# Kernel optimization log

Hardware: AMD Instinct MI355X
Metric: run time of the kernel (lower is better)

## Reference

```python
import jax, jax.numpy as jnp
import numpy as np

D = 120000   # sample_size
H1 = 600     # sample_size/200
H2 = 300     # sample_size/400
H3 = 200     # sample_size/600
DENSITY = 0.1  # sparselinear default connectivity
B = 512
EPS = 1e-5

_LAYER_SPECS = [(H1, D), (H1, H1), (H2, H1), (H3, H2), (H3, H3)]


def _make_idx(key, out_d, in_d, nnz):
    k1, k2 = jax.random.split(key)
    rows = jax.random.randint(k1, (nnz,), 0, out_d)
    cols = jax.random.randint(k2, (nnz,), 0, in_d)
    return jnp.stack([rows, cols]).astype(jnp.int32)


def setup_inputs() -> dict:
    key = jax.random.key(0)
    ks = jax.random.split(key, 32)
    inp = {"x": jax.random.normal(ks[0], (B, D), jnp.float32)}
    for i, (o, ii) in enumerate(_LAYER_SPECS, 1):
        nnz = int(DENSITY * o * ii)
        scale = 1.0 / np.sqrt(DENSITY * ii)  # kaiming-like fan-in scaling on nonzeros
        inp[f"idx{i}"] = _make_idx(ks[3 * i], o, ii, nnz)
        inp[f"val{i}"] = jax.random.normal(ks[3 * i + 1], (nnz,), jnp.float32) * scale
        inp[f"b{i}"] = jnp.zeros((o,), jnp.float32)
    for j, d in enumerate([H1, H2, H3], 1):
        inp[f"g{j}"] = jnp.ones((d,), jnp.float32)
        inp[f"be{j}"] = jnp.zeros((d,), jnp.float32)
    return inp


def _sp_linear(x, idx, vals, bias, out_d):
    # COO sparse linear: y = x @ W^T + b, W scattered from (row, col, val)
    in_d = x.shape[1]
    W = jnp.zeros((out_d, in_d), x.dtype).at[idx[0], idx[1]].add(vals)
    return x @ W.T + bias


def _bn(x, g, b):
    # BatchNorm1d, training mode: biased batch variance
    m = x.mean(axis=0)
    v = x.var(axis=0)
    return (x - m) * jax.lax.rsqrt(v + EPS) * g + b


def reference(x, idx1, val1, b1, idx2, val2, b2, idx3, val3, b3,
              idx4, val4, b4, idx5, val5, b5,
              g1, be1, g2, be2, g3, be3):
    h = jax.nn.silu(_bn(_sp_linear(x, idx1, val1, b1, H1), g1, be1))
    h = jax.nn.silu(_sp_linear(h, idx2, val2, b2, H1))
    h = jax.nn.silu(_bn(_sp_linear(h, idx3, val3, b3, H2), g2, be2))
    h = jax.nn.silu(_bn(_sp_linear(h, idx4, val4, b4, H3), g3, be3))
    return _sp_linear(h, idx5, val5, b5, H3)
```

## Files before the change

### kernel.cpp

```cpp
#include <hip/hip_runtime.h>

typedef unsigned short ushort_t;
typedef unsigned int uint_t;

typedef __bf16 bf16x8 __attribute__((ext_vector_type(8)));
typedef float  floatx4 __attribute__((ext_vector_type(4)));

#define AS3 __attribute__((address_space(3)))
#define AS1 __attribute__((address_space(1)))

#define BATCH 512
#define D_IN  120000
#define N1P   640
#define N2P   640
#define N3P   320
#define N4P   256
#define N5P   256

static constexpr long O_W1 = 0;
static constexpr long SZ_W1 = 640L * 120000 * 2;
static constexpr long O_W2 = O_W1 + SZ_W1;
static constexpr long SZ_W2 = 640L * 640 * 4;
static constexpr long O_W3 = O_W2 + SZ_W2;
static constexpr long SZ_W3 = 320L * 640 * 4;
static constexpr long O_W4 = O_W3 + SZ_W3;
static constexpr long SZ_W4 = 256L * 320 * 4;
static constexpr long O_W5 = O_W4 + SZ_W4;
static constexpr long SZ_W5 = 256L * 256 * 4;
static constexpr long O_Y1 = O_W5 + SZ_W5;
static constexpr long SZ_Y1 = 512L * 640 * 4;
static constexpr long ZERO_BYTES = O_Y1 + SZ_Y1;
static constexpr long O_XB = ZERO_BYTES;
static constexpr long SZ_XB = 512L * 120000 * 2;
static constexpr long O_H1 = O_XB;
static constexpr long O_H2 = O_H1 + 512L * 640 * 4;
static constexpr long O_Y3 = O_H2 + 512L * 640 * 4;
static constexpr long O_H3 = O_Y3 + 512L * 320 * 4;
static constexpr long O_Y4 = O_H3 + 512L * 320 * 4;
static constexpr long O_H4 = O_Y4 + 512L * 256 * 4;

__device__ __forceinline__ ushort_t f2bf(float f) {
    union { float f; uint_t u; } x;
    x.f = f;
    uint_t u = x.u;
    return (ushort_t)((u + 0x7FFFu + ((u >> 16) & 1u)) >> 16);
}
__device__ __forceinline__ float bf2f(ushort_t h) {
    union { uint_t u; float f; } x;
    x.u = ((uint_t)h) << 16;
    return x.f;
}
__device__ __forceinline__ float silu_f(float z) {
    return z / (1.f + expf(-z));
}
__device__ __forceinline__ void load16_lds(const void* g, void* l) {
    __builtin_amdgcn_global_load_lds((const AS1 char*)g, (AS3 char*)l, 16, 0, 0);
}

__global__ void zero_f4(float4* __restrict__ p, long n4) {
    long stride = (long)gridDim.x * blockDim.x;
    for (long i = (long)blockIdx.x * blockDim.x + threadIdx.x; i < n4; i += stride)
        p[i] = make_float4(0.f, 0.f, 0.f, 0.f);
}

__global__ void cast_f32_bf16(const float* __restrict__ X, ushort_t* __restrict__ Xb, long n8) {
    long t = (long)blockIdx.x * blockDim.x + threadIdx.x;
    if (t >= n8) return;
    const float4* p = (const float4*)X + 2 * t;
    float4 a = p[0], b = p[1];
    union { ushort_t us[8]; uint4 v; } u;
    u.us[0] = f2bf(a.x); u.us[1] = f2bf(a.y); u.us[2] = f2bf(a.z); u.us[3] = f2bf(a.w);
    u.us[4] = f2bf(b.x); u.us[5] = f2bf(b.y); u.us[6] = f2bf(b.z); u.us[7] = f2bf(b.w);
    ((uint4*)Xb)[t] = u.v;
}

__global__ void scatter_bf16(const int* __restrict__ idx, const float* __restrict__ vals,
                             int nnz, ushort_t* __restrict__ W, int ldw) {
    int i = blockIdx.x * blockDim.x + threadIdx.x;
    if (i >= nnz) return;
    int r = idx[i];
    int c = idx[nnz + i];
    float v = vals[i];
    size_t e = (size_t)r * ldw + c;
    uint_t* word = (uint_t*)((char*)W + ((e * 2) & ~(size_t)3));
    bool hi = (e & 1);
    uint_t cur = *word, assumed;
    do {
        assumed = cur;
        ushort_t h = hi ? (ushort_t)(assumed >> 16) : (ushort_t)(assumed & 0xFFFFu);
        ushort_t nh = f2bf(bf2f(h) + v);
        uint_t nw = hi ? ((assumed & 0x0000FFFFu) | ((uint_t)nh << 16))
                       : ((assumed & 0xFFFF0000u) | (uint_t)nh);
        cur = atomicCAS(word, assumed, nw);
    } while (cur != assumed);
}

__global__ void scatter_f32(const int* __restrict__ idx, const float* __restrict__ vals,
                            int nnz, float* __restrict__ W, int ldw) {
    int i = blockIdx.x * blockDim.x + threadIdx.x;
    if (i >= nnz) return;
    atomicAdd(&W[(size_t)idx[i] * ldw + idx[nnz + i]], vals[i]);
}

__global__ __launch_bounds__(256) void gemm1(const ushort_t* __restrict__ X,
                                             const ushort_t* __restrict__ W,
                                             float* __restrict__ Y, int kChunk) {
    __shared__ ushort_t sA[128 * 32];
    __shared__ ushort_t sB[128 * 32];

    const int tile = blockIdx.x;
    const int bm = tile / 5, bn = tile % 5;
    const int ks = blockIdx.y * kChunk;
    const int iters = kChunk / 32;

    const int t = threadIdx.x;
    const int lane = t & 63;
    const int w = t >> 6;
    const int wm = w >> 1, wn = w & 1;

    const int c0 = w * 128 + lane;
    const int c1 = c0 + 64;
    const int rA0 = c0 >> 2, qA0 = c0 & 3;
    const int rA1 = c1 >> 2, qA1 = c1 & 3;

    const ushort_t* pa0 = X + (size_t)(bm * 128 + rA0) * D_IN + ks + qA0 * 8;
    const ushort_t* pa1 = X + (size_t)(bm * 128 + rA1) * D_IN + ks + qA1 * 8;
    const ushort_t* pb0 = W + (size_t)(bn * 128 + rA0) * D_IN + ks + qA0 * 8;
    const ushort_t* pb1 = W + (size_t)(bn * 128 + rA1) * D_IN + ks + qA1 * 8;

    ushort_t* la0 = sA + (size_t)(w * 128) * 8;
    ushort_t* la1 = sA + (size_t)(w * 128 + 64) * 8;
    ushort_t* lb0 = sB + (size_t)(w * 128) * 8;
    ushort_t* lb1 = sB + (size_t)(w * 128 + 64) * 8;

    const int i16 = lane & 15;
    const int qk = lane >> 4;
    const bf16x8* ap[4];
    const bf16x8* bp[4];
#pragma unroll
    for (int mi = 0; mi < 4; mi++)
        ap[mi] = (const bf16x8*)&sA[(size_t)(wm * 64 + mi * 16 + i16) * 32 + qk * 8];
#pragma unroll
    for (int ni = 0; ni < 4; ni++)
        bp[ni] = (const bf16x8*)&sB[(size_t)(wn * 64 + ni * 16 + i16) * 32 + qk * 8];

    floatx4 acc[4][4] = {};

    for (int it = 0; it < iters; ++it) {
        __syncthreads();
        load16_lds(pa0, la0);
        load16_lds(pa1, la1);
        load16_lds(pb0, lb0);
        load16_lds(pb1, lb1);
        pa0 += 32; pa1 += 32; pb0 += 32; pb1 += 32;
        __syncthreads();

        bf16x8 af[4], bfr[4];
#pragma unroll
        for (int mi = 0; mi < 4; mi++) af[mi] = *ap[mi];
#pragma unroll
        for (int ni = 0; ni < 4; ni++) bfr[ni] = *bp[ni];
#pragma unroll
        for (int mi = 0; mi < 4; mi++)
#pragma unroll
            for (int ni = 0; ni < 4; ni++)
                acc[mi][ni] = __builtin_amdgcn_mfma_f32_16x16x32_bf16(af[mi], bfr[ni], acc[mi][ni], 0, 0, 0);
    }

#pragma unroll
    for (int mi = 0; mi < 4; mi++) {
#pragma unroll
        for (int ni = 0; ni < 4; ni++) {
#pragma unroll
            for (int r = 0; r < 4; r++) {
                int row = bm * 128 + wm * 64 + mi * 16 + qk * 4 + r;
                int col = bn * 128 + wn * 64 + ni * 16 + i16;
                atomicAdd(&Y[(size_t)row * N1P + col], acc[mi][ni][r]);
            }
        }
    }
}

__global__ void bn_silu(const float* __restrict__ Y, int ld, int realN,
                        const float* __restrict__ g, const float* __restrict__ be,
                        float* __restrict__ H) {
    int j = blockIdx.x;
    int t = threadIdx.x;
    if (j >= realN) {
        for (int b = t; b < BATCH; b += 256) H[(size_t)b * ld + j] = 0.f;
        return;
    }
    float v0 = Y[(size_t)t * ld + j];
    float v1 = Y[(size_t)(t + 256) * ld + j];
    __shared__ float rs[256], rss[256];
    rs[t] = v0 + v1;
    rss[t] = v0 * v0 + v1 * v1;
    __syncthreads();
    for (int o = 128; o > 0; o >>= 1) {
        if (t < o) { rs[t] += rs[t + o]; rss[t] += rss[t + o]; }
        __syncthreads();
    }
    float mean = rs[0] * (1.f / 512.f);
    float var  = rss[0] * (1.f / 512.f) - mean * mean;
    float sc = rsqrtf(var + 1e-5f) * g[j];
    float sh = be[j] - mean * sc;
    H[(size_t)t * ld + j]         = silu_f(v0 * sc + sh);
    H[(size_t)(t + 256) * ld + j] = silu_f(v1 * sc + sh);
}

template <int ACT, int GUARD>
__global__ __launch_bounds__(256) void small_gemm(const float* __restrict__ A, int lda,
                                                  const float* __restrict__ W, int ldw,
                                                  const float* __restrict__ bias, int biasN,
                                                  float* __restrict__ out, int ldo, int outN,
                                                  int K) {
    __shared__ float sA[64][20];
    __shared__ float sB[64][20];
    const int t = threadIdx.x;
    const int m0 = blockIdx.x * 64, n0 = blockIdx.y * 64;
    const int ty = t >> 4, tx = t & 15;
    const int lm = t >> 2, lq = t & 3;
    float acc[4][4] = {};

    for (int kt = 0; kt < K; kt += 16) {
        __syncthreads();
        float4 av = *(const float4*)&A[(size_t)(m0 + lm) * lda + kt + lq * 4];
        float4 wv = *(const float4*)&W[(size_t)(n0 + lm) * ldw + kt + lq * 4];
        sA[lm][lq * 4 + 0] = av.x; sA[lm][lq * 4 + 1] = av.y;
        sA[lm][lq * 4 + 2] = av.z; sA[lm][lq * 4 + 3] = av.w;
        sB[lm][lq * 4 + 0] = wv.x; sB[lm][lq * 4 + 1] = wv.y;
        sB[lm][lq * 4 + 2] = wv.z; sB[lm][lq * 4 + 3] = wv.w;
        __syncthreads();
#pragma unroll
        for (int kg = 0; kg < 4; kg++) {
            float4 a4[4], b4[4];
#pragma unroll
            for (int i = 0; i < 4; i++) a4[i] = *(const float4*)&sA[ty * 4 + i][kg * 4];
#pragma unroll
            for (int j = 0; j < 4; j++) b4[j] = *(const float4*)&sB[tx * 4 + j][kg * 4];
#pragma unroll
            for (int i = 0; i < 4; i++)
#pragma unroll
                for (int j = 0; j < 4; j++)
                    acc[i][j] += a4[i].x * b4[j].x + a4[i].y * b4[j].y +
                                 a4[i].z * b4[j].z + a4[i].w * b4[j].w;
        }
    }

#pragma unroll
    for (int i = 0; i < 4; i++) {
#pragma unroll
        for (int j = 0; j < 4; j++) {
            int row = m0 + ty * 4 + i;
            int col = n0 + tx * 4 + j;
            float v = acc[i][j];
            if (bias != nullptr && col < biasN) v += bias[col];
            if (ACT == 1) v = silu_f(v);
            if (GUARD) {
                if (col < outN) out[(size_t)row * ldo + col] = v;
            } else {
                out[(size_t)row * ldo + col] = v;
            }
        }
    }
}

extern "C" void kernel_launch(void* const* d_in, const int* in_sizes, int n_in,
                              void* d_out, int out_size, void* d_ws, size_t ws_size,
                              hipStream_t stream) {
    const float* x   = (const float*)d_in[0];
    const int* idx1 = (const int*)d_in[1];  const float* val1 = (const float*)d_in[2];
    const int* idx2 = (const int*)d_in[4];  const float* val2 = (const float*)d_in[5];
    const float* b2 = (const float*)d_in[6];
    const int* idx3 = (const int*)d_in[7];  const float* val3 = (const float*)d_in[8];
    const int* idx4 = (const int*)d_in[10]; const float* val4 = (const float*)d_in[11];
    const int* idx5 = (const int*)d_in[13]; const float* val5 = (const float*)d_in[14];
    const float* b5 = (const float*)d_in[15];
    const float* g1 = (const float*)d_in[16]; const float* be1 = (const float*)d_in[17];
    const float* g2 = (const float*)d_in[18]; const float* be2 = (const float*)d_in[19];
    const float* g3 = (const float*)d_in[20]; const float* be3 = (const float*)d_in[21];

    const int nnz1 = in_sizes[1] / 2;
    const int nnz2 = in_sizes[4] / 2;
    const int nnz3 = in_sizes[7] / 2;
    const int nnz4 = in_sizes[10] / 2;
    const int nnz5 = in_sizes[13] / 2;

    char* ws = (char*)d_ws;
    ushort_t* W1 = (ushort_t*)(ws + O_W1);
    float* W2 = (float*)(ws + O_W2);
    float* W3 = (float*)(ws + O_W3);
    float* W4 = (float*)(ws + O_W4);
    float* W5 = (float*)(ws + O_W5);
    float* y1 = (float*)(ws + O_Y1);
    ushort_t* Xb = (ushort_t*)(ws + O_XB);
    float* h1 = (float*)(ws + O_H1);
    float* h2 = (float*)(ws + O_H2);
    float* y3 = (float*)(ws + O_Y3);
    float* h3 = (float*)(ws + O_H3);
    float* y4 = (float*)(ws + O_Y4);
    float* h4 = (float*)(ws + O_H4);

    zero_f4<<<dim3(2048), dim3(256), 0, stream>>>((float4*)ws, ZERO_BYTES / 16);

    {
        long n8 = (long)BATCH * D_IN / 8;
        cast_f32_bf16<<<dim3((unsigned)((n8 + 255) / 256)), dim3(256), 0, stream>>>(x, Xb, n8);
    }

    scatter_bf16<<<dim3((nnz1 + 255) / 256), dim3(256), 0, stream>>>(idx1, val1, nnz1, W1, D_IN);
    scatter_f32<<<dim3((nnz2 + 255) / 256), dim3(256), 0, stream>>>(idx2, val2, nnz2, W2, 640);
    scatter_f32<<<dim3((nnz3 + 255) / 256), dim3(256), 0, stream>>>(idx3, val3, nnz3, W3, 640);
    scatter_f32<<<dim3((nnz4 + 255) / 256), dim3(256), 0, stream>>>(idx4, val4, nnz4, W4, 320);
    scatter_f32<<<dim3((nnz5 + 255) / 256), dim3(256), 0, stream>>>(idx5, val5, nnz5, W5, 256);

    gemm1<<<dim3(20, 30), dim3(256), 0, stream>>>(Xb, W1, y1, 4000);

    bn_silu<<<dim3(N1P), dim3(256), 0, stream>>>(y1, N1P, 600, g1, be1, h1);

    small_gemm<1, 0><<<dim3(8, N2P / 64), dim3(256), 0, stream>>>(h1, N1P, W2, 640, b2, 600,
                                                                  h2, N2P, N2P, 640);
    small_gemm<0, 0><<<dim3(8, N3P / 64), dim3(256), 0, stream>>>(h2, N2P, W3, 640, nullptr, 0,
                                                                  y3, N3P, N3P, 640);
    bn_silu<<<dim3(N3P), dim3(256), 0, stream>>>(y3, N3P, 300, g2, be2, h3);

    small_gemm<0, 0><<<dim3(8, N4P / 64), dim3(256), 0, stream>>>(h3, N3P, W4, 320, nullptr, 0,
                                                                  y4, N4P, N4P, 320);
    bn_silu<<<dim3(N4P), dim3(256), 0, stream>>>(y4, N4P, 200, g3, be3, h4);

    small_gemm<0, 1><<<dim3(8, N5P / 64), dim3(256), 0, stream>>>(h4, N4P, W5, 256, b5, 200,
                                                                  (float*)d_out, 200, 200, 256);
    (void)n_in; (void)out_size; (void)ws_size;
}
```

Before: 1.174 ms.

## Build W1 from row/column buckets in LDS instead of CAS-scattering bf16

```diff
diff --git a/kernel.cpp b/kernel.cpp
--- a/kernel.cpp
+++ b/kernel.cpp
@@ -16,6 +16,12 @@
 #define N3P   320
 #define N4P   256
 #define N5P   256
+
+#define QSH   14
+#define QW    (1 << QSH)
+#define NQ    8
+#define BCAP  2048
+#define NBUCK (600 * NQ)
 
 static constexpr long O_W1 = 0;
 static constexpr long SZ_W1 = 640L * 120000 * 2;
@@ -27,11 +33,16 @@
 static constexpr long SZ_W4 = 256L * 320 * 4;
 static constexpr long O_W5 = O_W4 + SZ_W4;
 static constexpr long SZ_W5 = 256L * 256 * 4;
-static constexpr long O_Y1 = O_W5 + SZ_W5;
+static constexpr long O_CUR = O_W5 + SZ_W5;
+static constexpr long SZ_CUR = 640L * 8 * 4;
+static constexpr long O_Y1 = O_CUR + SZ_CUR;
 static constexpr long SZ_Y1 = 512L * 640 * 4;
-static constexpr long ZERO_BYTES = O_Y1 + SZ_Y1;
-static constexpr long O_XB = ZERO_BYTES;
+static constexpr long ZERO_OFF = O_W2;
+static constexpr long ZERO_BYTES = (O_Y1 + SZ_Y1) - O_W2;
+static constexpr long O_XB = O_Y1 + SZ_Y1;
 static constexpr long SZ_XB = 512L * 120000 * 2;
+static constexpr long O_BC = O_XB;
+static constexpr long O_BV = O_BC + (long)NBUCK * BCAP * 4;
 static constexpr long O_H1 = O_XB;
 static constexpr long O_H2 = O_H1 + 512L * 640 * 4;
 static constexpr long O_Y3 = O_H2 + 512L * 640 * 4;
@@ -44,11 +55,6 @@
     x.f = f;
     uint_t u = x.u;
     return (ushort_t)((u + 0x7FFFu + ((u >> 16) & 1u)) >> 16);
-}
-__device__ __forceinline__ float bf2f(ushort_t h) {
-    union { uint_t u; float f; } x;
-    x.u = ((uint_t)h) << 16;
-    return x.f;
 }
 __device__ __forceinline__ float silu_f(float z) {
     return z / (1.f + expf(-z));
@@ -74,25 +80,60 @@
     ((uint4*)Xb)[t] = u.v;
 }
 
-__global__ void scatter_bf16(const int* __restrict__ idx, const float* __restrict__ vals,
-                             int nnz, ushort_t* __restrict__ W, int ldw) {
+__global__ void reorder1(const int* __restrict__ idx, const float* __restrict__ vals,
+                         int nnz, int* __restrict__ cur,
+                         int* __restrict__ bcol, float* __restrict__ bval) {
     int i = blockIdx.x * blockDim.x + threadIdx.x;
     if (i >= nnz) return;
     int r = idx[i];
     int c = idx[nnz + i];
-    float v = vals[i];
-    size_t e = (size_t)r * ldw + c;
-    uint_t* word = (uint_t*)((char*)W + ((e * 2) & ~(size_t)3));
-    bool hi = (e & 1);
-    uint_t cur = *word, assumed;
-    do {
-        assumed = cur;
-        ushort_t h = hi ? (ushort_t)(assumed >> 16) : (ushort_t)(assumed & 0xFFFFu);
-        ushort_t nh = f2bf(bf2f(h) + v);
-        uint_t nw = hi ? ((assumed & 0x0000FFFFu) | ((uint_t)nh << 16))
-                       : ((assumed & 0xFFFF0000u) | (uint_t)nh);
-        cur = atomicCAS(word, assumed, nw);
-    } while (cur != assumed);
+    int b = r * NQ + (c >> QSH);
+    int off = atomicAdd(&cur[b], 1);
+    if (off < BCAP) {
+        long p = (long)b * BCAP + off;
+        bcol[p] = c;
+        bval[p] = vals[i];
+    }
+}
+
+__global__ __launch_bounds__(256) void build_w1(const int* __restrict__ bcol,
+                                                const float* __restrict__ bval,
+                                                const int* __restrict__ cnt,
+                                                ushort_t* __restrict__ W) {
+    const int bid = blockIdx.x;
+    const int r = bid >> 3, q = bid & 7;
+    const int t = threadIdx.x;
+    const int c0 = q << QSH;
+    const int ncols = min(QW, D_IN - c0);
+    ushort_t* dst = W + (size_t)r * D_IN + c0;
+
+    if (r >= 600) {
+        uint4 z = make_uint4(0, 0, 0, 0);
+        for (int j = t * 8; j < ncols; j += 256 * 8)
+            *(uint4*)(dst + j) = z;
+        return;
+    }
+
+    __shared__ float sm[QW];
+    for (int j = t * 4; j < QW; j += 256 * 4)
+        *(float4*)&sm[j] = make_float4(0.f, 0.f, 0.f, 0.f);
+    __syncthreads();
+
+    const int b = r * NQ + q;
+    int n = cnt[b];
+    if (n > BCAP) n = BCAP;
+    const int* pc = bcol + (long)b * BCAP;
+    const float* pv = bval + (long)b * BCAP;
+    for (int i = t; i < n; i += 256)
+        atomicAdd(&sm[pc[i] & (QW - 1)], pv[i]);
+    __syncthreads();
+
+    for (int j = t * 8; j < ncols; j += 256 * 8) {
+        union { ushort_t us[8]; uint4 v; } u;
+#pragma unroll
+        for (int k = 0; k < 8; k++) u.us[k] = f2bf(sm[j + k]);
+        *(uint4*)(dst + j) = u.v;
+    }
 }
 
 __global__ void scatter_f32(const int* __restrict__ idx, const float* __restrict__ vals,
@@ -292,7 +333,10 @@
     float* W3 = (float*)(ws + O_W3);
     float* W4 = (float*)(ws + O_W4);
     float* W5 = (float*)(ws + O_W5);
+    int*   cur = (int*)(ws + O_CUR);
     float* y1 = (float*)(ws + O_Y1);
+    int*   bc = (int*)(ws + O_BC);
+    float* bv = (float*)(ws + O_BV);
     ushort_t* Xb = (ushort_t*)(ws + O_XB);
     float* h1 = (float*)(ws + O_H1);
     float* h2 = (float*)(ws + O_H2);
@@ -301,14 +345,18 @@
     float* y4 = (float*)(ws + O_Y4);
     float* h4 = (float*)(ws + O_H4);
 
-    zero_f4<<<dim3(2048), dim3(256), 0, stream>>>((float4*)ws, ZERO_BYTES / 16);
+    zero_f4<<<dim3((unsigned)(ZERO_BYTES / 16 / 256 + 1)), dim3(256), 0, stream>>>(
+        (float4*)(ws + ZERO_OFF), ZERO_BYTES / 16);
+
+    reorder1<<<dim3((nnz1 + 255) / 256), dim3(256), 0, stream>>>(idx1, val1, nnz1, cur, bc, bv);
+
+    build_w1<<<dim3(640 * NQ), dim3(256), 0, stream>>>(bc, bv, cur, W1);
 
     {
         long n8 = (long)BATCH * D_IN / 8;
         cast_f32_bf16<<<dim3((unsigned)((n8 + 255) / 256)), dim3(256), 0, stream>>>(x, Xb, n8);
     }
 
-    scatter_bf16<<<dim3((nnz1 + 255) / 256), dim3(256), 0, stream>>>(idx1, val1, nnz1, W1, D_IN);
     scatter_f32<<<dim3((nnz2 + 255) / 256), dim3(256), 0, stream>>>(idx2, val2, nnz2, W2, 640);
     scatter_f32<<<dim3((nnz3 + 255) / 256), dim3(256), 0, stream>>>(idx3, val3, nnz3, W3, 640);
     scatter_f32<<<dim3((nnz4 + 255) / 256), dim3(256), 0, stream>>>(idx4, val4, nnz4, W4, 320);
```

After: 1.306 ms. 11.3% more time.
